# Optimization experiments

Hardware: AMD Instinct MI355X
Metric: run time of the kernel (lower is better)

Reference implementation:

```python
import jax, jax.numpy as jnp
import numpy as np

N_NODES = 50000
N_EDGES = 800000
IN_DIM = 128
HID = 32
HEADS = 4
EMB = 64
NEG_SLOPE = 0.2
LN_EPS = 1e-5


def setup_inputs() -> dict:
    key = jax.random.key(0)
    ks = jax.random.split(key, 16)
    s = 0.1
    inp = {
        'x': jax.random.normal(ks[0], (N_NODES, IN_DIM), dtype=jnp.float32),
        'edge_index': jax.random.randint(ks[1], (2, N_EDGES), 0, N_NODES, dtype=jnp.int64),
        # GATConv 1: in=128 -> heads=4, out_per_head=32, concat -> 128
        'W1': jax.random.normal(ks[2], (IN_DIM, HEADS * HID), dtype=jnp.float32) * s,
        'att_src1': jax.random.normal(ks[3], (HEADS, HID), dtype=jnp.float32) * s,
        'att_dst1': jax.random.normal(ks[4], (HEADS, HID), dtype=jnp.float32) * s,
        'b1': jnp.zeros((HEADS * HID,), dtype=jnp.float32),
        'gamma1': jnp.ones((HEADS * HID,), dtype=jnp.float32),
        'beta1': jnp.zeros((HEADS * HID,), dtype=jnp.float32),
        # GATConv 2: in=128 -> heads=1, out=64, concat=False
        'W2': jax.random.normal(ks[5], (HEADS * HID, EMB), dtype=jnp.float32) * s,
        'att_src2': jax.random.normal(ks[6], (1, EMB), dtype=jnp.float32) * s,
        'att_dst2': jax.random.normal(ks[7], (1, EMB), dtype=jnp.float32) * s,
        'b2': jnp.zeros((EMB,), dtype=jnp.float32),
        'gamma2': jnp.ones((EMB,), dtype=jnp.float32),
        'beta2': jnp.zeros((EMB,), dtype=jnp.float32),
    }
    return inp


def _gat_conv(x, src, dst, W, att_src, att_dst):
    # x: [N, F_in]; src/dst: [E'] (self loops included); W: [F_in, H*C]
    N = x.shape[0]
    H, C = att_src.shape
    h = (x @ W).reshape(N, H, C)                          # [N, H, C]
    a_s = jnp.sum(h * att_src, axis=-1)                   # [N, H]
    a_d = jnp.sum(h * att_dst, axis=-1)                   # [N, H]
    e = jax.nn.leaky_relu(a_s[src] + a_d[dst], NEG_SLOPE) # [E', H]
    # segment softmax over destination-node neighborhoods
    m = jax.ops.segment_max(e, dst, num_segments=N)       # [N, H]
    ex = jnp.exp(e - m[dst])
    den = jax.ops.segment_sum(ex, dst, num_segments=N)    # [N, H]
    alpha = ex / den[dst]                                  # [E', H]
    msg = h[src] * alpha[:, :, None]                       # [E', H, C]
    return jax.ops.segment_sum(msg, dst, num_segments=N)  # [N, H, C]


def _layer_norm(x, gamma, beta):
    mu = jnp.mean(x, axis=-1, keepdims=True)
    var = jnp.var(x, axis=-1, keepdims=True)
    return (x - mu) * jax.lax.rsqrt(var + LN_EPS) * gamma + beta


def reference(x, edge_index, W1, att_src1, att_dst1, b1, gamma1, beta1,
              W2, att_src2, att_dst2, b2, gamma2, beta2):
    N = x.shape[0]
    loops = jnp.arange(N, dtype=edge_index.dtype)
    src = jnp.concatenate([edge_index[0], loops])  # PyG add_self_loops=True
    dst = jnp.concatenate([edge_index[1], loops])

    # gat1: heads=4, concat=True
    h1 = _gat_conv(x, src, dst, W1, att_src1, att_dst1)   # [N, 4, 32]
    h1 = h1.reshape(N, -1) + b1                            # [N, 128]
    h1 = jax.nn.relu(_layer_norm(h1, gamma1, beta1))
    # dropout is identity in eval mode

    # gat2: heads=1, concat=False (mean over the single head)
    h2 = _gat_conv(h1, src, dst, W2, att_src2, att_dst2)  # [N, 1, 64]
    h2 = h2.mean(axis=1) + b2                              # [N, 64]
    return _layer_norm(h2, gamma2, beta2)
```

## Files before the change

kernel.cpp:

```cpp
#include <hip/hip_runtime.h>
#include <hip/hip_bf16.h>
#include <math.h>

#define N_NODES 50000
#define N_EDGES 800000
#define HEADS 4
#define HID 32
#define D1 128
#define D2 64
#define NEG_SLOPE 0.2f
#define LN_EPS 1e-5f

#define NB_SCAN ((N_NODES + 255) / 256)
#define CAP 64
#define GB1 ((N_NODES + 127) / 128)
#define DEGB 784

__device__ __forceinline__ float lrelu(float x) { return x > 0.f ? x : NEG_SLOPE * x; }
__device__ __forceinline__ float bf2f(__hip_bfloat16 v) { return __bfloat162float(v); }

__global__ __launch_bounds__(256) void gemm1_att1_degree_kernel(
    const float* __restrict__ X, const float* __restrict__ W,
    __hip_bfloat16* __restrict__ Y,
    const float* __restrict__ att_src, const float* __restrict__ att_dst,
    float* __restrict__ a_s, float* __restrict__ a_d,
    const int* __restrict__ dst, int* __restrict__ deg, int* __restrict__ rank) {
    if (blockIdx.x >= GB1) {
        int t0 = (blockIdx.x - GB1) * 256 + threadIdx.x;
        const int stride = DEGB * 256;
#pragma unroll
        for (int u = 0; u < 4; ++u) {
            int i = t0 + u * stride;
            if (i < N_EDGES) rank[i] = atomicAdd(&deg[dst[i]], 1);
        }
        return;
    }
    constexpr int COLS = 128;
    constexpr int CG = 8, RPT = 4;
    __shared__ float Wlds[128 * COLS];
    for (int i = threadIdx.x; i < 128 * COLS; i += 256) Wlds[i] = W[i];
    __syncthreads();

    int cg = threadIdx.x % CG;
    int rg = threadIdx.x / CG;
    int r0 = blockIdx.x * 128 + rg * RPT;
    int c0 = cg * 16;

    float acc[RPT][16];
#pragma unroll
    for (int i = 0; i < RPT; ++i)
#pragma unroll
        for (int j = 0; j < 16; ++j) acc[i][j] = 0.f;

    const float* xrow[RPT];
#pragma unroll
    for (int i = 0; i < RPT; ++i) {
        int ri = r0 + i;
        if (ri >= N_NODES) ri = N_NODES - 1;
        xrow[i] = X + (size_t)ri * 128;
    }

    for (int k = 0; k < 128; k += 4) {
        float4 xv[RPT];
#pragma unroll
        for (int i = 0; i < RPT; ++i) xv[i] = *(const float4*)&xrow[i][k];
#pragma unroll
        for (int kk = 0; kk < 4; ++kk) {
            const float* wrow = &Wlds[(k + kk) * COLS + c0];
            const float4 w0 = *(const float4*)(wrow + 0);
            const float4 w1 = *(const float4*)(wrow + 4);
            const float4 w2 = *(const float4*)(wrow + 8);
            const float4 w3 = *(const float4*)(wrow + 12);
#pragma unroll
            for (int i = 0; i < RPT; ++i) {
                float xk = (kk == 0) ? xv[i].x : (kk == 1) ? xv[i].y : (kk == 2) ? xv[i].z : xv[i].w;
                acc[i][0]  += xk * w0.x; acc[i][1]  += xk * w0.y;
                acc[i][2]  += xk * w0.z; acc[i][3]  += xk * w0.w;
                acc[i][4]  += xk * w1.x; acc[i][5]  += xk * w1.y;
                acc[i][6]  += xk * w1.z; acc[i][7]  += xk * w1.w;
                acc[i][8]  += xk * w2.x; acc[i][9]  += xk * w2.y;
                acc[i][10] += xk * w2.z; acc[i][11] += xk * w2.w;
                acc[i][12] += xk * w3.x; acc[i][13] += xk * w3.y;
                acc[i][14] += xk * w3.z; acc[i][15] += xk * w3.w;
            }
        }
    }

    int head = cg >> 1;
    int half = cg & 1;
    float asv[16], adv[16];
#pragma unroll
    for (int j = 0; j < 16; ++j) {
        asv[j] = att_src[head * 32 + half * 16 + j];
        adv[j] = att_dst[head * 32 + half * 16 + j];
    }
#pragma unroll
    for (int i = 0; i < RPT; ++i) {
        int r = r0 + i;
        float ps = 0.f, pd = 0.f;
#pragma unroll
        for (int j = 0; j < 16; ++j) {
            ps += acc[i][j] * asv[j];
            pd += acc[i][j] * adv[j];
        }
        ps += __shfl_xor(ps, 1, 64);
        pd += __shfl_xor(pd, 1, 64);
        if (r < N_NODES) {
            __hip_bfloat162* yp = (__hip_bfloat162*)(Y + (size_t)r * COLS + c0);
#pragma unroll
            for (int j = 0; j < 8; ++j) {
                __hip_bfloat162 p;
                p.x = __float2bfloat16(acc[i][2 * j]);
                p.y = __float2bfloat16(acc[i][2 * j + 1]);
                yp[j] = p;
            }
            if (half == 0) {
                a_s[r * 4 + head] = ps;
                a_d[r * 4 + head] = pd;
            }
        }
    }
}

__global__ __launch_bounds__(256) void scan1_kernel(const int* __restrict__ deg,
                                                    int* __restrict__ rpl,
                                                    int* __restrict__ bsum) {
    int i = blockIdx.x * 256 + threadIdx.x;
    int v = (i < N_NODES) ? deg[i] : 0;
    int lane = threadIdx.x & 63;
    int w = threadIdx.x >> 6;
    int x = v;
#pragma unroll
    for (int off = 1; off < 64; off <<= 1) {
        int t = __shfl_up(x, off, 64);
        if (lane >= off) x += t;
    }
    __shared__ int wsum[4];
    if (lane == 63) wsum[w] = x;
    __syncthreads();
    int wo = 0;
    if (w > 0) wo += wsum[0];
    if (w > 1) wo += wsum[1];
    if (w > 2) wo += wsum[2];
    if (i <= N_NODES) rpl[i] = x - v + wo;
    if (threadIdx.x == 255) bsum[blockIdx.x] = x + wo;
}

__global__ __launch_bounds__(256) void scan2_kernel(const int* __restrict__ bsum,
                                                    int* __restrict__ boff) {
    int i = threadIdx.x;
    int v = (i < NB_SCAN) ? bsum[i] : 0;
    int lane = threadIdx.x & 63;
    int w = threadIdx.x >> 6;
    int x = v;
#pragma unroll
    for (int off = 1; off < 64; off <<= 1) {
        int t = __shfl_up(x, off, 64);
        if (lane >= off) x += t;
    }
    __shared__ int wsum[4];
    if (lane == 63) wsum[w] = x;
    __syncthreads();
    int wo = 0;
    if (w > 0) wo += wsum[0];
    if (w > 1) wo += wsum[1];
    if (w > 2) wo += wsum[2];
    if (i < NB_SCAN) boff[i] = x - v + wo;
}

__global__ __launch_bounds__(256) void scatter_kernel(const int* __restrict__ src,
                                                      const int* __restrict__ dst,
                                                      const int* __restrict__ rpl,
                                                      const int* __restrict__ boff,
                                                      const int* __restrict__ rank,
                                                      int* __restrict__ col) {
    int i = blockIdx.x * blockDim.x + threadIdx.x;
    if (i < N_EDGES) {
        int d = dst[i];
        int pos = rpl[d] + boff[d >> 8] + rank[i];
        col[pos] = src[i];
    }
}

__global__ __launch_bounds__(256) void agg1_kernel(const __hip_bfloat16* __restrict__ h,
                                                   const float* __restrict__ a_s,
                                                   const float* __restrict__ a_d,
                                                   const int* __restrict__ rpl,
                                                   const int* __restrict__ boff,
                                                   const int* __restrict__ col,
                                                   const float* __restrict__ b1,
                                                   const float* __restrict__ gamma,
                                                   const float* __restrict__ beta,
                                                   float* __restrict__ out) {
    __shared__ int colsh[4][CAP];
    __shared__ float wsh[4][CAP * 4];
    int wv = threadIdx.x >> 6;
    int lane = threadIdx.x & 63;
    int n = blockIdx.x * 4 + wv;
    int nn = (n < N_NODES) ? n : N_NODES - 1;
    int head = lane >> 4;
    int c = 2 * lane;

    const float4 ad4 = *(const float4*)&a_d[nn * 4];
    int beg = rpl[nn] + boff[nn >> 8];
    int end = rpl[nn + 1] + boff[(nn + 1) >> 8];
    int deg = end - beg;

    float den0 = 0.f, den1 = 0.f, den2 = 0.f, den3 = 0.f;
    for (int t = lane; t < deg; t += 64) {
        int s = col[beg + t];
        const float4 as4 = *(const float4*)&a_s[s * 4];
        float w0 = __expf(lrelu(as4.x + ad4.x));
        float w1 = __expf(lrelu(as4.y + ad4.y));
        float w2 = __expf(lrelu(as4.z + ad4.z));
        float w3 = __expf(lrelu(as4.w + ad4.w));
        if (t < CAP) {
            colsh[wv][t] = s;
            *(float4*)&wsh[wv][t * 4] = make_float4(w0, w1, w2, w3);
        }
        den0 += w0; den1 += w1; den2 += w2; den3 += w3;
    }
#pragma unroll
    for (int m = 1; m < 64; m <<= 1) {
        den0 += __shfl_xor(den0, m, 64);
        den1 += __shfl_xor(den1, m, 64);
        den2 += __shfl_xor(den2, m, 64);
        den3 += __shfl_xor(den3, m, 64);
    }
    float adh = (head == 0) ? ad4.x : (head == 1) ? ad4.y : (head == 2) ? ad4.z : ad4.w;
    float wself = __expf(lrelu(a_s[nn * 4 + head] + adh));
    float den = ((head == 0) ? den0 : (head == 1) ? den1 : (head == 2) ? den2 : den3) + wself;

    __syncthreads();

    float ax0 = 0.f, ay0 = 0.f, ax1 = 0.f, ay1 = 0.f;
    int m0 = (deg < CAP) ? deg : CAP;
    int j = 0;
    for (; j + 3 < m0; j += 4) {
        int s0 = colsh[wv][j + 0], s1 = colsh[wv][j + 1];
        int s2 = colsh[wv][j + 2], s3 = colsh[wv][j + 3];
        float w0 = wsh[wv][(j + 0) * 4 + head], w1 = wsh[wv][(j + 1) * 4 + head];
        float w2 = wsh[wv][(j + 2) * 4 + head], w3 = wsh[wv][(j + 3) * 4 + head];
        __hip_bfloat162 h0 = ((const __hip_bfloat162*)h)[(size_t)s0 * 64 + lane];
        __hip_bfloat162 h1 = ((const __hip_bfloat162*)h)[(size_t)s1 * 64 + lane];
        __hip_bfloat162 h2v = ((const __hip_bfloat162*)h)[(size_t)s2 * 64 + lane];
        __hip_bfloat162 h3 = ((const __hip_bfloat162*)h)[(size_t)s3 * 64 + lane];
        ax0 += w0 * bf2f(h0.x); ay0 += w0 * bf2f(h0.y);
        ax1 += w1 * bf2f(h1.x); ay1 += w1 * bf2f(h1.y);
        ax0 += w2 * bf2f(h2v.x); ay0 += w2 * bf2f(h2v.y);
        ax1 += w3 * bf2f(h3.x); ay1 += w3 * bf2f(h3.y);
    }
    for (; j < m0; ++j) {
        int s = colsh[wv][j];
        float w = wsh[wv][j * 4 + head];
        __hip_bfloat162 hv = ((const __hip_bfloat162*)h)[(size_t)s * 64 + lane];
        ax0 += w * bf2f(hv.x); ay0 += w * bf2f(hv.y);
    }
    for (; j < deg; ++j) {
        int s = col[beg + j];
        float w = __expf(lrelu(a_s[s * 4 + head] + adh));
        __hip_bfloat162 hv = ((const __hip_bfloat162*)h)[(size_t)s * 64 + lane];
        ax0 += w * bf2f(hv.x); ay0 += w * bf2f(hv.y);
    }
    {
        __hip_bfloat162 hv = ((const __hip_bfloat162*)h)[(size_t)nn * 64 + lane];
        ax0 += wself * bf2f(hv.x); ay0 += wself * bf2f(hv.y);
    }
    float inv = 1.f / den;
    float vx = (ax0 + ax1) * inv + b1[c];
    float vy = (ay0 + ay1) * inv + b1[c + 1];

    float s1 = vx + vy, s2 = vx * vx + vy * vy;
#pragma unroll
    for (int m = 1; m < 64; m <<= 1) {
        s1 += __shfl_xor(s1, m, 64);
        s2 += __shfl_xor(s2, m, 64);
    }
    float mean = s1 * (1.f / 128.f);
    float var = s2 * (1.f / 128.f) - mean * mean;
    float r = rsqrtf(var + LN_EPS);
    float ox = fmaxf(0.f, (vx - mean) * r * gamma[c] + beta[c]);
    float oy = fmaxf(0.f, (vy - mean) * r * gamma[c + 1] + beta[c + 1]);
    if (n < N_NODES) *(float2*)&out[(size_t)n * 128 + c] = make_float2(ox, oy);
}

__global__ __launch_bounds__(256) void gemm2_att2_kernel(const float* __restrict__ X,
                                                         const float* __restrict__ W,
                                                         __hip_bfloat16* __restrict__ Y,
                                                         const float* __restrict__ att_src,
                                                         const float* __restrict__ att_dst,
                                                         float* __restrict__ a_s,
                                                         float* __restrict__ a_d) {
    constexpr int COLS = 64;
    constexpr int CG = 4, RPT = 2;
    __shared__ float Wlds[128 * COLS];
    for (int i = threadIdx.x; i < 128 * COLS; i += 256) Wlds[i] = W[i];
    __syncthreads();

    int cg = threadIdx.x % CG;
    int rg = threadIdx.x / CG;
    int r0 = blockIdx.x * 128 + rg * RPT;
    int c0 = cg * 16;

    float acc[RPT][16];
#pragma unroll
    for (int i = 0; i < RPT; ++i)
#pragma unroll
        for (int j = 0; j < 16; ++j) acc[i][j] = 0.f;

    const float* xrow[RPT];
#pragma unroll
    for (int i = 0; i < RPT; ++i) {
        int ri = r0 + i;
        if (ri >= N_NODES) ri = N_NODES - 1;
        xrow[i] = X + (size_t)ri * 128;
    }

    for (int k = 0; k < 128; k += 4) {
        float4 xv[RPT];
#pragma unroll
        for (int i = 0; i < RPT; ++i) xv[i] = *(const float4*)&xrow[i][k];
#pragma unroll
        for (int kk = 0; kk < 4; ++kk) {
            const float* wrow = &Wlds[(k + kk) * COLS + c0];
            const float4 w0 = *(const float4*)(wrow + 0);
            const float4 w1 = *(const float4*)(wrow + 4);
            const float4 w2 = *(const float4*)(wrow + 8);
            const float4 w3 = *(const float4*)(wrow + 12);
#pragma unroll
            for (int i = 0; i < RPT; ++i) {
                float xk = (kk == 0) ? xv[i].x : (kk == 1) ? xv[i].y : (kk == 2) ? xv[i].z : xv[i].w;
                acc[i][0]  += xk * w0.x; acc[i][1]  += xk * w0.y;
                acc[i][2]  += xk * w0.z; acc[i][3]  += xk * w0.w;
                acc[i][4]  += xk * w1.x; acc[i][5]  += xk * w1.y;
                acc[i][6]  += xk * w1.z; acc[i][7]  += xk * w1.w;
                acc[i][8]  += xk * w2.x; acc[i][9]  += xk * w2.y;
                acc[i][10] += xk * w2.z; acc[i][11] += xk * w2.w;
                acc[i][12] += xk * w3.x; acc[i][13] += xk * w3.y;
                acc[i][14] += xk * w3.z; acc[i][15] += xk * w3.w;
            }
        }
    }

    float asv[16], adv[16];
#pragma unroll
    for (int j = 0; j < 16; ++j) {
        asv[j] = att_src[c0 + j];
        adv[j] = att_dst[c0 + j];
    }
#pragma unroll
    for (int i = 0; i < RPT; ++i) {
        int r = r0 + i;
        float ps = 0.f, pd = 0.f;
#pragma unroll
        for (int j = 0; j < 16; ++j) {
            ps += acc[i][j] * asv[j];
            pd += acc[i][j] * adv[j];
        }
        ps += __shfl_xor(ps, 1, 64);
        pd += __shfl_xor(pd, 1, 64);
        ps += __shfl_xor(ps, 2, 64);
        pd += __shfl_xor(pd, 2, 64);
        if (r < N_NODES) {
            __hip_bfloat162* yp = (__hip_bfloat162*)(Y + (size_t)r * COLS + c0);
#pragma unroll
            for (int j = 0; j < 8; ++j) {
                __hip_bfloat162 p;
                p.x = __float2bfloat16(acc[i][2 * j]);
                p.y = __float2bfloat16(acc[i][2 * j + 1]);
                yp[j] = p;
            }
            if (cg == 0) {
                a_s[r] = ps;
                a_d[r] = pd;
            }
        }
    }
}

__global__ __launch_bounds__(256) void agg2_kernel(const __hip_bfloat16* __restrict__ h,
                                                   const float* __restrict__ a_s,
                                                   const float* __restrict__ a_d,
                                                   const int* __restrict__ rpl,
                                                   const int* __restrict__ boff,
                                                   const int* __restrict__ col,
                                                   const float* __restrict__ b2,
                                                   const float* __restrict__ gamma,
                                                   const float* __restrict__ beta,
                                                   float* __restrict__ out) {
    __shared__ int colsh[4][CAP];
    __shared__ float wsh[4][CAP];
    int wv = threadIdx.x >> 6;
    int lane = threadIdx.x & 63;
    int n = blockIdx.x * 4 + wv;
    int nn = (n < N_NODES) ? n : N_NODES - 1;

    float adh = a_d[nn];
    int beg = rpl[nn] + boff[nn >> 8];
    int end = rpl[nn + 1] + boff[(nn + 1) >> 8];
    int deg = end - beg;

    float den = 0.f;
    for (int t = lane; t < deg; t += 64) {
        int s = col[beg + t];
        float w = __expf(lrelu(a_s[s] + adh));
        if (t < CAP) {
            colsh[wv][t] = s;
            wsh[wv][t] = w;
        }
        den += w;
    }
#pragma unroll
    for (int m = 1; m < 64; m <<= 1) den += __shfl_xor(den, m, 64);
    float wself = __expf(lrelu(a_s[nn] + adh));
    den += wself;

    __syncthreads();

    float a0 = 0.f, a1 = 0.f;
    int m0 = (deg < CAP) ? deg : CAP;
    int j = 0;
    for (; j + 3 < m0; j += 4) {
        int s0 = colsh[wv][j + 0], s1 = colsh[wv][j + 1];
        int s2 = colsh[wv][j + 2], s3 = colsh[wv][j + 3];
        float w0 = wsh[wv][j + 0], w1 = wsh[wv][j + 1];
        float w2 = wsh[wv][j + 2], w3 = wsh[wv][j + 3];
        a0 += w0 * bf2f(h[(size_t)s0 * 64 + lane]);
        a1 += w1 * bf2f(h[(size_t)s1 * 64 + lane]);
        a0 += w2 * bf2f(h[(size_t)s2 * 64 + lane]);
        a1 += w3 * bf2f(h[(size_t)s3 * 64 + lane]);
    }
    for (; j < m0; ++j) {
        a0 += wsh[wv][j] * bf2f(h[(size_t)colsh[wv][j] * 64 + lane]);
    }
    for (; j < deg; ++j) {
        int s = col[beg + j];
        float w = __expf(lrelu(a_s[s] + adh));
        a0 += w * bf2f(h[(size_t)s * 64 + lane]);
    }
    a0 += wself * bf2f(h[(size_t)nn * 64 + lane]);

    float v = (a0 + a1) / den + b2[lane];

    float s1 = v, s2 = v * v;
#pragma unroll
    for (int m = 1; m < 64; m <<= 1) {
        s1 += __shfl_xor(s1, m, 64);
        s2 += __shfl_xor(s2, m, 64);
    }
    float mean = s1 * (1.f / 64.f);
    float var = s2 * (1.f / 64.f) - mean * mean;
    float r = rsqrtf(var + LN_EPS);
    if (n < N_NODES) out[(size_t)n * 64 + lane] = (v - mean) * r * gamma[lane] + beta[lane];
}

extern "C" void kernel_launch(void* const* d_in, const int* in_sizes, int n_in,
                              void* d_out, int out_size, void* d_ws, size_t ws_size,
                              hipStream_t stream) {
    const float* x        = (const float*)d_in[0];
    const int*   ei       = (const int*)d_in[1];
    const float* W1       = (const float*)d_in[2];
    const float* att_src1 = (const float*)d_in[3];
    const float* att_dst1 = (const float*)d_in[4];
    const float* b1       = (const float*)d_in[5];
    const float* gamma1   = (const float*)d_in[6];
    const float* beta1    = (const float*)d_in[7];
    const float* W2       = (const float*)d_in[8];
    const float* att_src2 = (const float*)d_in[9];
    const float* att_dst2 = (const float*)d_in[10];
    const float* b2       = (const float*)d_in[11];
    const float* gamma2   = (const float*)d_in[12];
    const float* beta2    = (const float*)d_in[13];
    const int* src = ei;
    const int* dst = ei + N_EDGES;
    float* out = (float*)d_out;

    char* ws = (char*)d_ws;
    size_t off = 0;
    auto alloc = [&](size_t bytes) -> void* {
        void* p = ws + off;
        off += bytes;
        off = (off + 255) & ~(size_t)255;
        return p;
    };
    __hip_bfloat16* h1pre = (__hip_bfloat16*)alloc((size_t)N_NODES * 128 * 2);
    __hip_bfloat16* h2pre = (__hip_bfloat16*)alloc((size_t)N_NODES * 64 * 2);
    float* a_s1   = (float*)alloc((size_t)N_NODES * 4 * 4);
    float* a_d1   = (float*)alloc((size_t)N_NODES * 4 * 4);
    float* h1n    = (float*)alloc((size_t)N_NODES * 128 * 4);
    float* a_s2   = (float*)alloc((size_t)N_NODES * 4);
    float* a_d2   = (float*)alloc((size_t)N_NODES * 4);
    int* deg      = (int*)alloc((size_t)N_NODES * 4);
    int* rpl      = (int*)alloc((size_t)(N_NODES + 1) * 4);
    int* col      = (int*)alloc((size_t)N_EDGES * 4);
    int* rank     = (int*)alloc((size_t)N_EDGES * 4);
    int* bsum     = (int*)alloc((size_t)NB_SCAN * 4);
    int* boff     = (int*)alloc((size_t)NB_SCAN * 4);

    hipMemsetAsync(deg, 0, (size_t)N_NODES * 4, stream);

    const int EB = (N_EDGES + 255) / 256;
    const int NWB = (N_NODES + 3) / 4;

    gemm1_att1_degree_kernel<<<GB1 + DEGB, 256, 0, stream>>>(
        x, W1, h1pre, att_src1, att_dst1, a_s1, a_d1, dst, deg, rank);
    scan1_kernel<<<NB_SCAN, 256, 0, stream>>>(deg, rpl, bsum);
    scan2_kernel<<<1, 256, 0, stream>>>(bsum, boff);
    scatter_kernel<<<EB, 256, 0, stream>>>(src, dst, rpl, boff, rank, col);

    agg1_kernel<<<NWB, 256, 0, stream>>>(h1pre, a_s1, a_d1, rpl, boff, col, b1, gamma1, beta1, h1n);

    gemm2_att2_kernel<<<(N_NODES + 127) / 128, 256, 0, stream>>>(
        h1n, W2, h2pre, att_src2, att_dst2, a_s2, a_d2);
    agg2_kernel<<<NWB, 256, 0, stream>>>(h2pre, a_s2, a_d2, rpl, boff, col, b2, gamma2, beta2, out);
}
```

Baseline: 252.7 us.

## Move node GEMMs to bf16 MFMA with hi/lo split for fp32 accuracy

Replaces the scalar-FMA LDS-tiled GEMMs for both GAT layers with MFMA 16x16x32 bf16 kernels. Each fp32 operand is split into bf16 hi and lo parts and three MFMA products are summed to keep near-fp32 precision. A small prep kernel pre-splits and pre-swizzles W1/W2 into MFMA fragment layout, so weights load straight into registers with no LDS staging. GEMM blocks and degree-counting blocks are interleaved in the fused launch to overlap atomic work with compute. This adds one extra launch and per-element split arithmetic on X.

```diff
diff --git a/kernel.cpp b/kernel.cpp
--- a/kernel.cpp
+++ b/kernel.cpp
@@ -13,20 +13,77 @@
 
 #define NB_SCAN ((N_NODES + 255) / 256)
 #define CAP 64
-#define GB1 ((N_NODES + 127) / 128)
+#define GB1N 782
+#define GB2N 782
 #define DEGB 784
+#define ILV (2 * GB1N)
+
+typedef __attribute__((ext_vector_type(8))) short bf16x8;
+typedef __attribute__((ext_vector_type(4))) float f32x4;
 
 __device__ __forceinline__ float lrelu(float x) { return x > 0.f ? x : NEG_SLOPE * x; }
 __device__ __forceinline__ float bf2f(__hip_bfloat16 v) { return __bfloat162float(v); }
 
-__global__ __launch_bounds__(256) void gemm1_att1_degree_kernel(
-    const float* __restrict__ X, const float* __restrict__ W,
+__device__ __forceinline__ short f2bf_s(float x) {
+    union { __hip_bfloat16 h; short s; } u;
+    u.h = __float2bfloat16(x);
+    return u.s;
+}
+__device__ __forceinline__ float bfs2f(short s) {
+    union { unsigned u; float f; } v;
+    v.u = ((unsigned)(unsigned short)s) << 16;
+    return v.f;
+}
+__device__ __forceinline__ void split_bf(float x, short& hi, short& lo) {
+    hi = f2bf_s(x);
+    lo = f2bf_s(x - bfs2f(hi));
+}
+
+__global__ __launch_bounds__(256) void wprep_kernel(const float* __restrict__ W1,
+                                                    const float* __restrict__ W2,
+                                                    short* __restrict__ W1h, short* __restrict__ W1l,
+                                                    short* __restrict__ W2h, short* __restrict__ W2l) {
+    int idx = blockIdx.x * 256 + threadIdx.x;
+    if (idx < 16384) {
+        int s = idx & 7, l = (idx >> 3) & 63, fid = idx >> 9;
+        int kt = fid & 3, nt = fid >> 2;
+        int k = kt * 32 + (l >> 4) * 8 + s;
+        int n = nt * 16 + (l & 15);
+        short hi, lo;
+        split_bf(W1[k * 128 + n], hi, lo);
+        W1h[idx] = hi;
+        W1l[idx] = lo;
+    } else if (idx < 16384 + 8192) {
+        int j = idx - 16384;
+        int s = j & 7, l = (j >> 3) & 63, fid = j >> 9;
+        int kt = fid & 3, nt = fid >> 2;
+        int k = kt * 32 + (l >> 4) * 8 + s;
+        int n = nt * 16 + (l & 15);
+        short hi, lo;
+        split_bf(W2[k * 64 + n], hi, lo);
+        W2h[j] = hi;
+        W2l[j] = lo;
+    }
+}
+
+__global__ __launch_bounds__(256, 3) void gemm1_mfma_degree_kernel(
+    const float* __restrict__ X, const short* __restrict__ Wh, const short* __restrict__ Wl,
     __hip_bfloat16* __restrict__ Y,
     const float* __restrict__ att_src, const float* __restrict__ att_dst,
     float* __restrict__ a_s, float* __restrict__ a_d,
     const int* __restrict__ dst, int* __restrict__ deg, int* __restrict__ rank) {
-    if (blockIdx.x >= GB1) {
-        int t0 = (blockIdx.x - GB1) * 256 + threadIdx.x;
+    int bid = blockIdx.x;
+    bool isdeg;
+    int id;
+    if (bid < ILV) {
+        isdeg = (bid & 1);
+        id = bid >> 1;
+    } else {
+        isdeg = true;
+        id = bid - ILV + GB1N;
+    }
+    if (isdeg) {
+        int t0 = id * 256 + threadIdx.x;
         const int stride = DEGB * 256;
 #pragma unroll
         for (int u = 0; u < 4; ++u) {
@@ -35,89 +92,163 @@
         }
         return;
     }
-    constexpr int COLS = 128;
-    constexpr int CG = 8, RPT = 4;
-    __shared__ float Wlds[128 * COLS];
-    for (int i = threadIdx.x; i < 128 * COLS; i += 256) Wlds[i] = W[i];
+
+    int tid = threadIdx.x;
+    int w = tid >> 6;
+    int l = tid & 63;
+    int lr = l & 15;
+    int lq = l >> 4;
+
+    const bf16x8* Wh8 = (const bf16x8*)Wh;
+    const bf16x8* Wl8 = (const bf16x8*)Wl;
+    bf16x8 bh[2][4], bl[2][4];
+#pragma unroll
+    for (int nt = 0; nt < 2; ++nt)
+#pragma unroll
+        for (int kt = 0; kt < 4; ++kt) {
+            int fid = (2 * w + nt) * 4 + kt;
+            bh[nt][kt] = Wh8[fid * 64 + l];
+            bl[nt][kt] = Wl8[fid * 64 + l];
+        }
+
+    int r0 = id * 64;
+    float asv0 = att_src[w * 32 + lr], asv1 = att_src[w * 32 + 16 + lr];
+    float adv0 = att_dst[w * 32 + lr], adv1 = att_dst[w * 32 + 16 + lr];
+
+#pragma unroll
+    for (int mt = 0; mt < 4; ++mt) {
+        int rb = r0 + mt * 16;
+        int row = rb + lr;
+        if (row >= N_NODES) row = N_NODES - 1;
+        const float* xr = X + (size_t)row * 128;
+        f32x4 acc0 = {0.f, 0.f, 0.f, 0.f};
+        f32x4 acc1 = {0.f, 0.f, 0.f, 0.f};
+#pragma unroll
+        for (int kt = 0; kt < 4; ++kt) {
+            int cb = kt * 32 + lq * 8;
+            float4 f0 = *(const float4*)(xr + cb);
+            float4 f1 = *(const float4*)(xr + cb + 4);
+            float xs[8] = {f0.x, f0.y, f0.z, f0.w, f1.x, f1.y, f1.z, f1.w};
+            bf16x8 ah, al;
+#pragma unroll
+            for (int s = 0; s < 8; ++s) {
+                short h_, l_;
+                split_bf(xs[s], h_, l_);
+                ah[s] = h_;
+                al[s] = l_;
+            }
+            acc0 = __builtin_amdgcn_mfma_f32_16x16x32_bf16(ah, bh[0][kt], acc0, 0, 0, 0);
+            acc1 = __builtin_amdgcn_mfma_f32_16x16x32_bf16(ah, bh[1][kt], acc1, 0, 0, 0);
+            acc0 = __builtin_amdgcn_mfma_f32_16x16x32_bf16(al, bh[0][kt], acc0, 0, 0, 0);
+            acc1 = __builtin_amdgcn_mfma_f32_16x16x32_bf16(al, bh[1][kt], acc1, 0, 0, 0);
+            acc0 = __builtin_amdgcn_mfma_f32_16x16x32_bf16(ah, bl[0][kt], acc0, 0, 0, 0);
+            acc1 = __builtin_amdgcn_mfma_f32_16x16x32_bf16(ah, bl[1][kt], acc1, 0, 0, 0);
+        }
+#pragma unroll
+        for (int reg = 0; reg < 4; ++reg) {
+            int r = rb + lq * 4 + reg;
+            float v0 = acc0[reg], v1 = acc1[reg];
+            float ps = v0 * asv0 + v1 * asv1;
+            float pd = v0 * adv0 + v1 * adv1;
+#pragma unroll
+            for (int m = 1; m < 16; m <<= 1) {
+                ps += __shfl_xor(ps, m, 64);
+                pd += __shfl_xor(pd, m, 64);
+            }
+            if (r < N_NODES) {
+                Y[(size_t)r * 128 + w * 32 + lr] = __float2bfloat16(v0);
+                Y[(size_t)r * 128 + w * 32 + 16 + lr] = __float2bfloat16(v1);
+                if (lr == 0) {
+                    a_s[r * 4 + w] = ps;
+                    a_d[r * 4 + w] = pd;
+                }
+            }
+        }
+    }
+}
+
+__global__ __launch_bounds__(256, 3) void gemm2_mfma_kernel(
+    const float* __restrict__ X, const short* __restrict__ Wh, const short* __restrict__ Wl,
+    __hip_bfloat16* __restrict__ Y,
+    const float* __restrict__ att_src, const float* __restrict__ att_dst,
+    float* __restrict__ a_s, float* __restrict__ a_d) {
+    __shared__ float psh[4][64];
+    __shared__ float pdh[4][64];
+    int tid = threadIdx.x;
+    int w = tid >> 6;
+    int l = tid & 63;
+    int lr = l & 15;
+    int lq = l >> 4;
+
+    const bf16x8* Wh8 = (const bf16x8*)Wh;
+    const bf16x8* Wl8 = (const bf16x8*)Wl;
+    bf16x8 bh[4], bl[4];
+#pragma unroll
+    for (int kt = 0; kt < 4; ++kt) {
+        int fid = w * 4 + kt;
+        bh[kt] = Wh8[fid * 64 + l];
+        bl[kt] = Wl8[fid * 64 + l];
+    }
+
+    int r0 = blockIdx.x * 64;
+    float asv = att_src[w * 16 + lr];
+    float adv = att_dst[w * 16 + lr];
+
+    f32x4 acc[4];
+#pragma unroll
+    for (int mt = 0; mt < 4; ++mt) acc[mt] = (f32x4){0.f, 0.f, 0.f, 0.f};
+
+#pragma unroll
+    for (int mt = 0; mt < 4; ++mt) {
+        int row = r0 + mt * 16 + lr;
+        if (row >= N_NODES) row = N_NODES - 1;
+        const float* xr = X + (size_t)row * 128;
+#pragma unroll
+        for (int kt = 0; kt < 4; ++kt) {
+            int cb = kt * 32 + lq * 8;
+            float4 f0 = *(const float4*)(xr + cb);
+            float4 f1 = *(const float4*)(xr + cb + 4);
+            float xs[8] = {f0.x, f0.y, f0.z, f0.w, f1.x, f1.y, f1.z, f1.w};
+            bf16x8 ah, al;
+#pragma unroll
+            for (int s = 0; s < 8; ++s) {
+                short h_, l_;
+                split_bf(xs[s], h_, l_);
+                ah[s] = h_;
+                al[s] = l_;
+            }
+            acc[mt] = __builtin_amdgcn_mfma_f32_16x16x32_bf16(ah, bh[kt], acc[mt], 0, 0, 0);
+            acc[mt] = __builtin_amdgcn_mfma_f32_16x16x32_bf16(al, bh[kt], acc[mt], 0, 0, 0);
+            acc[mt] = __builtin_amdgcn_mfma_f32_16x16x32_bf16(ah, bl[kt], acc[mt], 0, 0, 0);
+        }
+    }
+
+#pragma unroll
+    for (int mt = 0; mt < 4; ++mt) {
+#pragma unroll
+        for (int reg = 0; reg < 4; ++reg) {
+            int r = r0 + mt * 16 + lq * 4 + reg;
+            float v = acc[mt][reg];
+            float ps = v * asv;
+            float pd = v * adv;
+#pragma unroll
+            for (int m = 1; m < 16; m <<= 1) {
+                ps += __shfl_xor(ps, m, 64);
+                pd += __shfl_xor(pd, m, 64);
+            }
+            if (r < N_NODES) Y[(size_t)r * 64 + w * 16 + lr] = __float2bfloat16(v);
+            if (lr == 0) {
+                psh[w][mt * 16 + lq * 4 + reg] = ps;
+                pdh[w][mt * 16 + lq * 4 + reg] = pd;
+            }
+        }
+    }
     __syncthreads();
-
-    int cg = threadIdx.x % CG;
-    int rg = threadIdx.x / CG;
-    int r0 = blockIdx.x * 128 + rg * RPT;
-    int c0 = cg * 16;
-
-    float acc[RPT][16];
-#pragma unroll
-    for (int i = 0; i < RPT; ++i)
-#pragma unroll
-        for (int j = 0; j < 16; ++j) acc[i][j] = 0.f;
-
-    const float* xrow[RPT];
-#pragma unroll
-    for (int i = 0; i < RPT; ++i) {
-        int ri = r0 + i;
-        if (ri >= N_NODES) ri = N_NODES - 1;
-        xrow[i] = X + (size_t)ri * 128;
-    }
-
-    for (int k = 0; k < 128; k += 4) {
-        float4 xv[RPT];
-#pragma unroll
-        for (int i = 0; i < RPT; ++i) xv[i] = *(const float4*)&xrow[i][k];
-#pragma unroll
-        for (int kk = 0; kk < 4; ++kk) {
-            const float* wrow = &Wlds[(k + kk) * COLS + c0];
-            const float4 w0 = *(const float4*)(wrow + 0);
-            const float4 w1 = *(const float4*)(wrow + 4);
-            const float4 w2 = *(const float4*)(wrow + 8);
-            const float4 w3 = *(const float4*)(wrow + 12);
-#pragma unroll
-            for (int i = 0; i < RPT; ++i) {
-                float xk = (kk == 0) ? xv[i].x : (kk == 1) ? xv[i].y : (kk == 2) ? xv[i].z : xv[i].w;
-                acc[i][0]  += xk * w0.x; acc[i][1]  += xk * w0.y;
-                acc[i][2]  += xk * w0.z; acc[i][3]  += xk * w0.w;
-                acc[i][4]  += xk * w1.x; acc[i][5]  += xk * w1.y;
-                acc[i][6]  += xk * w1.z; acc[i][7]  += xk * w1.w;
-                acc[i][8]  += xk * w2.x; acc[i][9]  += xk * w2.y;
-                acc[i][10] += xk * w2.z; acc[i][11] += xk * w2.w;
-                acc[i][12] += xk * w3.x; acc[i][13] += xk * w3.y;
-                acc[i][14] += xk * w3.z; acc[i][15] += xk * w3.w;
-            }
-        }
-    }
-
-    int head = cg >> 1;
-    int half = cg & 1;
-    float asv[16], adv[16];
-#pragma unroll
-    for (int j = 0; j < 16; ++j) {
-        asv[j] = att_src[head * 32 + half * 16 + j];
-        adv[j] = att_dst[head * 32 + half * 16 + j];
-    }
-#pragma unroll
-    for (int i = 0; i < RPT; ++i) {
-        int r = r0 + i;
-        float ps = 0.f, pd = 0.f;
-#pragma unroll
-        for (int j = 0; j < 16; ++j) {
-            ps += acc[i][j] * asv[j];
-            pd += acc[i][j] * adv[j];
-        }
-        ps += __shfl_xor(ps, 1, 64);
-        pd += __shfl_xor(pd, 1, 64);
+    if (tid < 64) {
+        int r = r0 + tid;
         if (r < N_NODES) {
-            __hip_bfloat162* yp = (__hip_bfloat162*)(Y + (size_t)r * COLS + c0);
-#pragma unroll
-            for (int j = 0; j < 8; ++j) {
-                __hip_bfloat162 p;
-                p.x = __float2bfloat16(acc[i][2 * j]);
-                p.y = __float2bfloat16(acc[i][2 * j + 1]);
-                yp[j] = p;
-            }
-            if (half == 0) {
-                a_s[r * 4 + head] = ps;
-                a_d[r * 4 + head] = pd;
-            }
+            a_s[r] = psh[0][tid] + psh[1][tid] + psh[2][tid] + psh[3][tid];
+            a_d[r] = pdh[0][tid] + pdh[1][tid] + pdh[2][tid] + pdh[3][tid];
         }
     }
 }
@@ -282,100 +413,6 @@
     float ox = fmaxf(0.f, (vx - mean) * r * gamma[c] + beta[c]);
     float oy = fmaxf(0.f, (vy - mean) * r * gamma[c + 1] + beta[c + 1]);
     if (n < N_NODES) *(float2*)&out[(size_t)n * 128 + c] = make_float2(ox, oy);
-}
-
-__global__ __launch_bounds__(256) void gemm2_att2_kernel(const float* __restrict__ X,
-                                                         const float* __restrict__ W,
-                                                         __hip_bfloat16* __restrict__ Y,
-                                                         const float* __restrict__ att_src,
-                                                         const float* __restrict__ att_dst,
-                                                         float* __restrict__ a_s,
-                                                         float* __restrict__ a_d) {
-    constexpr int COLS = 64;
-    constexpr int CG = 4, RPT = 2;
-    __shared__ float Wlds[128 * COLS];
-    for (int i = threadIdx.x; i < 128 * COLS; i += 256) Wlds[i] = W[i];
-    __syncthreads();
-
-    int cg = threadIdx.x % CG;
-    int rg = threadIdx.x / CG;
-    int r0 = blockIdx.x * 128 + rg * RPT;
-    int c0 = cg * 16;
-
-    float acc[RPT][16];
-#pragma unroll
-    for (int i = 0; i < RPT; ++i)
-#pragma unroll
-        for (int j = 0; j < 16; ++j) acc[i][j] = 0.f;
-
-    const float* xrow[RPT];
-#pragma unroll
-    for (int i = 0; i < RPT; ++i) {
-        int ri = r0 + i;
-        if (ri >= N_NODES) ri = N_NODES - 1;
-        xrow[i] = X + (size_t)ri * 128;
-    }
-
-    for (int k = 0; k < 128; k += 4) {
-        float4 xv[RPT];
-#pragma unroll
-        for (int i = 0; i < RPT; ++i) xv[i] = *(const float4*)&xrow[i][k];
-#pragma unroll
-        for (int kk = 0; kk < 4; ++kk) {
-            const float* wrow = &Wlds[(k + kk) * COLS + c0];
-            const float4 w0 = *(const float4*)(wrow + 0);
-            const float4 w1 = *(const float4*)(wrow + 4);
-            const float4 w2 = *(const float4*)(wrow + 8);
-            const float4 w3 = *(const float4*)(wrow + 12);
-#pragma unroll
-            for (int i = 0; i < RPT; ++i) {
-                float xk = (kk == 0) ? xv[i].x : (kk == 1) ? xv[i].y : (kk == 2) ? xv[i].z : xv[i].w;
-                acc[i][0]  += xk * w0.x; acc[i][1]  += xk * w0.y;
-                acc[i][2]  += xk * w0.z; acc[i][3]  += xk * w0.w;
-                acc[i][4]  += xk * w1.x; acc[i][5]  += xk * w1.y;
-                acc[i][6]  += xk * w1.z; acc[i][7]  += xk * w1.w;
-                acc[i][8]  += xk * w2.x; acc[i][9]  += xk * w2.y;
-                acc[i][10] += xk * w2.z; acc[i][11] += xk * w2.w;
-                acc[i][12] += xk * w3.x; acc[i][13] += xk * w3.y;
-                acc[i][14] += xk * w3.z; acc[i][15] += xk * w3.w;
-            }
-        }
-    }
-
-    float asv[16], adv[16];
-#pragma unroll
-    for (int j = 0; j < 16; ++j) {
-        asv[j] = att_src[c0 + j];
-        adv[j] = att_dst[c0 + j];
-    }
-#pragma unroll
-    for (int i = 0; i < RPT; ++i) {
-        int r = r0 + i;
-        float ps = 0.f, pd = 0.f;
-#pragma unroll
-        for (int j = 0; j < 16; ++j) {
-            ps += acc[i][j] * asv[j];
-            pd += acc[i][j] * adv[j];
-        }
-        ps += __shfl_xor(ps, 1, 64);
-        pd += __shfl_xor(pd, 1, 64);
-        ps += __shfl_xor(ps, 2, 64);
-        pd += __shfl_xor(pd, 2, 64);
-        if (r < N_NODES) {
-            __hip_bfloat162* yp = (__hip_bfloat162*)(Y + (size_t)r * COLS + c0);
-#pragma unroll
-            for (int j = 0; j < 8; ++j) {
-                __hip_bfloat162 p;
-                p.x = __float2bfloat16(acc[i][2 * j]);
-                p.y = __float2bfloat16(acc[i][2 * j + 1]);
-                yp[j] = p;
-            }
-            if (cg == 0) {
-                a_s[r] = ps;
-                a_d[r] = pd;
-            }
-        }
-    }
 }
 
 __global__ __launch_bounds__(256) void agg2_kernel(const __hip_bfloat16* __restrict__ h,
@@ -496,21 +533,27 @@
     int* rank     = (int*)alloc((size_t)N_EDGES * 4);
     int* bsum     = (int*)alloc((size_t)NB_SCAN * 4);
     int* boff     = (int*)alloc((size_t)NB_SCAN * 4);
+    short* W1h    = (short*)alloc((size_t)16384 * 2);
+    short* W1l    = (short*)alloc((size_t)16384 * 2);
+    short* W2h    = (short*)alloc((size_t)8192 * 2);
+    short* W2l    = (short*)alloc((size_t)8192 * 2);
 
     hipMemsetAsync(deg, 0, (size_t)N_NODES * 4, stream);
 
     const int EB = (N_EDGES + 255) / 256;
     const int NWB = (N_NODES + 3) / 4;
 
-    gemm1_att1_degree_kernel<<<GB1 + DEGB, 256, 0, stream>>>(
-        x, W1, h1pre, att_src1, att_dst1, a_s1, a_d1, dst, deg, rank);
+    wprep_kernel<<<96, 256, 0, stream>>>(W1, W2, W1h, W1l, W2h, W2l);
+
+    gemm1_mfma_degree_kernel<<<GB1N + DEGB, 256, 0, stream>>>(
+        x, W1h, W1l, h1pre, att_src1, att_dst1, a_s1, a_d1, dst, deg, rank);
     scan1_kernel<<<NB_SCAN, 256, 0, stream>>>(deg, rpl, bsum);
     scan2_kernel<<<1, 256, 0, stream>>>(bsum, boff);
     scatter_kernel<<<EB, 256, 0, stream>>>(src, dst, rpl, boff, rank, col);
 
     agg1_kernel<<<NWB, 256, 0, stream>>>(h1pre, a_s1, a_d1, rpl, boff, col, b1, gamma1, beta1, h1n);
 
-    gemm2_att2_kernel<<<(N_NODES + 127) / 128, 256, 0, stream>>>(
-        h1n, W2, h2pre, att_src2, att_dst2, a_s2, a_d2);
+    gemm2_mfma_kernel<<<GB2N, 256, 0, stream>>>(
+        h1n, W2h, W2l, h2pre, att_src2, att_dst2, a_s2, a_d2);
     agg2_kernel<<<NWB, 256, 0, stream>>>(h2pre, a_s2, a_d2, rpl, boff, col, b2, gamma2, beta2, out);
 }
```

Result: no change. 249.6 us (-1.2%).
